# Kernel tuning notes

Hardware: AMD Instinct MI355X
Metric: run time of the kernel (lower is better)

The kernel has to match this reference:

```python
import jax, jax.numpy as jnp
import numpy as np

B, N, M = 64, 256, 16
H_A = 256
DMIN, DMAX, STEP = 0.0, 3.0, 0.2
N_FILTERS = 16  # arange(0, 3.0+0.2, 0.2) -> 16 gaussians, == h_b
N_CONV = 3
N_CLASSES = 6
IN_DIM = 2 * H_A + N_FILTERS  # 528
EPS = 1e-5


def _bn(x, gamma, beta):
    # BatchNorm1d in training mode: batch stats over all but last axis, biased var
    axes = tuple(range(x.ndim - 1))
    mu = jnp.mean(x, axis=axes, keepdims=True)
    var = jnp.var(x, axis=axes, keepdims=True)
    return (x - mu) * jax.lax.rsqrt(var + EPS) * gamma + beta


def setup_inputs() -> dict:
    key = jax.random.key(0)
    ks = jax.random.split(key, 10)
    nbr_adj_dist = jax.random.uniform(ks[0], (B, N, M), dtype=jnp.float32) * DMAX
    nbr_adj_list = jax.random.randint(ks[1], (B, N, M), 0, N, dtype=jnp.int32)
    emb_table = jax.random.normal(ks[2], (N, H_A), dtype=jnp.float32)
    s = 1.0 / np.sqrt(IN_DIM)
    W_full = jax.random.uniform(ks[3], (N_CONV, IN_DIM, 2 * H_A), minval=-s, maxval=s, dtype=jnp.float32)
    b_full = jax.random.uniform(ks[4], (N_CONV, 2 * H_A), minval=-s, maxval=s, dtype=jnp.float32)
    g_h = jnp.ones((N_CONV, 2 * H_A), jnp.float32)
    beta_h = jnp.zeros((N_CONV, 2 * H_A), jnp.float32)
    g_o = jnp.ones((N_CONV, H_A), jnp.float32)
    beta_o = jnp.zeros((N_CONV, H_A), jnp.float32)
    sc = 1.0 / np.sqrt(H_A)
    W_cls = jax.random.uniform(ks[5], (H_A, N_CLASSES), minval=-sc, maxval=sc, dtype=jnp.float32)
    b_cls = jax.random.uniform(ks[6], (N_CLASSES,), minval=-sc, maxval=sc, dtype=jnp.float32)
    return {"nbr_adj_dist": nbr_adj_dist, "nbr_adj_list": nbr_adj_list,
            "emb_table": emb_table, "W_full": W_full, "b_full": b_full,
            "g_h": g_h, "beta_h": beta_h, "g_o": g_o, "beta_o": beta_o,
            "W_cls": W_cls, "b_cls": b_cls}


def reference(nbr_adj_dist, nbr_adj_list, emb_table, W_full, b_full,
              g_h, beta_h, g_o, beta_o, W_cls, b_cls):
    # Gaussian distance expansion -> bond embedding [B,N,M,h_b]
    filters = jnp.arange(DMIN, DMAX + STEP, STEP, dtype=jnp.float32)
    nbr_emb = jnp.exp(-((nbr_adj_dist[..., None] - filters) ** 2) / (STEP ** 2))

    # atom embedding of arange(N), broadcast over batch -> [B,N,h_a]
    atom_emb = jnp.broadcast_to(emb_table[None], (B, N, H_A))

    idx = nbr_adj_list.reshape(B, N * M, 1)
    for l in range(N_CONV):
        # gather neighbor atom embeddings [B,N,M,h_a]
        atom_nbr = jnp.take_along_axis(atom_emb, idx, axis=1).reshape(B, N, M, H_A)
        self_emb = jnp.broadcast_to(atom_emb[:, :, None, :], (B, N, M, H_A))
        total = jnp.concatenate([self_emb, atom_nbr, nbr_emb], axis=-1)  # [B,N,M,528]
        z = jnp.einsum('bnmi,io->bnmo', total, W_full[l]) + b_full[l]
        z = _bn(z, g_h[l], beta_h[l])
        nbr_filter, nbr_core = jnp.split(z, 2, axis=-1)
        nbr_sumed = jnp.sum(jax.nn.sigmoid(nbr_filter) * jax.nn.relu(nbr_core), axis=2)
        nbr_sumed = _bn(nbr_sumed, g_o[l], beta_o[l])
        atom_emb = jax.nn.relu(atom_emb + nbr_sumed)

    atom_emb = jax.nn.relu(atom_emb)
    pooled = jnp.sum(atom_emb, axis=1) / N  # pooling by num_atoms
    logits = pooled @ W_cls + b_cls
    return jax.nn.softmax(logits, axis=-1)
```

## Files before the change

kernel.cpp:

```cpp
#include <hip/hip_runtime.h>
#include <math.h>

#define NB 64
#define NA 256
#define NM 16
#define HA 256
#define NF 16
#define NCONV 3
#define NCLS 6
#define EPSB 1e-5f

typedef __attribute__((ext_vector_type(8))) short short8v;
typedef __attribute__((ext_vector_type(4))) float f32x4;

__device__ __forceinline__ short f2bf(float x) {
  union { float f; unsigned u; } v; v.f = x;
  unsigned r = v.u + 0x7fff + ((v.u >> 16) & 1);
  return (short)(r >> 16);
}

__global__ void prep_weights(const float* __restrict__ Wf,
                             short* __restrict__ WT, short* __restrict__ W3bf) {
  int i = blockIdx.x * 256 + threadIdx.x;
  const int TOT1 = NCONV * 1024 * 256;
  if (i < TOT1) {
    int l = i / (1024 * 256);
    int r = i - l * (1024 * 256);
    int o = r >> 8, k = r & 255;
    float w = (o < 512) ? Wf[(l * 528 + k) * 512 + o]
                        : Wf[(l * 528 + 256 + k) * 512 + (o - 512)];
    WT[i] = f2bf(w);
  }
  const int TOT2 = NCONV * 512 * NF;
  if (i < TOT2) {
    int l = i / (512 * NF);
    int r = i - l * (512 * NF);
    int o = r >> 4, k = r & 15;
    W3bf[i] = f2bf(Wf[(l * 528 + 512 + k) * 512 + o]);
  }
}

__global__ void gauss_kernel(const float* __restrict__ dist, short* __restrict__ Gbf) {
  int i = blockIdx.x * 256 + threadIdx.x;
  int r = i >> 4, f = i & 15;
  float d = dist[r];
  float x = d - 0.2f * (float)f;
  Gbf[i] = f2bf(__expf(-x * x * 25.0f));
}

__global__ void init_atom(const float* __restrict__ emb, float* __restrict__ atom) {
  int i = blockIdx.x * 256 + threadIdx.x;
  atom[i] = emb[i & (NA * HA - 1)];
}

__global__ void emb_bf(const float* __restrict__ emb, short* __restrict__ ebf) {
  int i = blockIdx.x * 256 + threadIdx.x;
  ebf[i] = f2bf(emb[i]);
}

__global__ __launch_bounds__(256) void gemm_mfma(const short* __restrict__ Abf,
                                                 const short* __restrict__ WT,
                                                 float* __restrict__ C, int Mrows) {
  __shared__ short As[128][72];
  __shared__ short Bs[128][72];
  int t = threadIdx.x;
  int wave = t >> 6, lane = t & 63;
  int wr = wave >> 1, wc = wave & 1;
  int l16 = lane & 15, lhi = lane >> 4;

  int wg = blockIdx.x;
  int nRowBlocks = Mrows >> 7;
  int rowBlock, colBlock;
  if (nRowBlocks >= 8) {
    rowBlock = (wg & 7) + ((wg >> 6) << 3);
    colBlock = (wg >> 3) & 7;
  } else {
    rowBlock = wg % nRowBlocks;
    colBlock = wg / nRowBlocks;
  }
  int rowBase = rowBlock << 7, colBase = colBlock << 7;

  f32x4 acc[4][4];
#pragma unroll
  for (int i = 0; i < 4; ++i)
#pragma unroll
    for (int j = 0; j < 4; ++j) acc[i][j] = (f32x4)(0.f);

  for (int k0 = 0; k0 < 256; k0 += 64) {
#pragma unroll
    for (int cc = 0; cc < 4; ++cc) {
      int c = t + cc * 256;
      int row = c >> 3, ko = (c & 7) << 3;
      *(int4*)&As[row][ko] = *(const int4*)&Abf[(size_t)(rowBase + row) * 256 + k0 + ko];
      *(int4*)&Bs[row][ko] = *(const int4*)&WT[(size_t)(colBase + row) * 256 + k0 + ko];
    }
    __syncthreads();
#pragma unroll
    for (int ks = 0; ks < 2; ++ks) {
      int kk = ks * 32 + lhi * 8;
      short8v a[4], b[4];
#pragma unroll
      for (int f = 0; f < 4; ++f) {
        a[f] = *(const short8v*)&As[wr * 64 + f * 16 + l16][kk];
        b[f] = *(const short8v*)&Bs[wc * 64 + f * 16 + l16][kk];
      }
#pragma unroll
      for (int i = 0; i < 4; ++i)
#pragma unroll
        for (int j = 0; j < 4; ++j)
          acc[i][j] = __builtin_amdgcn_mfma_f32_16x16x32_bf16(a[i], b[j], acc[i][j], 0, 0, 0);
    }
    __syncthreads();
  }
#pragma unroll
  for (int i = 0; i < 4; ++i) {
#pragma unroll
    for (int j = 0; j < 4; ++j) {
      int col = colBase + wc * 64 + j * 16 + l16;
      int row0 = rowBase + wr * 64 + i * 16 + lhi * 4;
#pragma unroll
      for (int r = 0; r < 4; ++r)
        C[(size_t)(row0 + r) * 1024 + col] = acc[i][j][r];
    }
  }
}

__device__ __forceinline__ void decode_wg(int wg, int& b, int& n0) {
  int x = wg & 7;
  int t2 = wg >> 3;
  int ng = t2 & 31;
  int bhi = t2 >> 5;
  b = bhi * 8 + x;
  n0 = ng * 8;
}

template <int PASS>
__global__ __launch_bounds__(256, 2) void pass_mfma(const float* __restrict__ H,
                                                    const short* __restrict__ Gbf,
                                                    const int* __restrict__ adj,
                                                    const short* __restrict__ W3bf,
                                                    const float* __restrict__ coef,
                                                    float* __restrict__ nbr,
                                                    float* __restrict__ stats,
                                                    int batched) {
  __shared__ short Gb[128][40];
  __shared__ short W3t[512][40];
  __shared__ float x1s[8][512];
  __shared__ int jis[128];
  __shared__ float cf[1024];

  int t = threadIdx.x;
  int b, n0;
  decode_wg(blockIdx.x, b, n0);
  int hbase = batched ? b * NA : 0;

#pragma unroll
  for (int c = 0; c < 2; ++c) {
    int col = t * 2 + c;
    const int4* src = (const int4*)&W3bf[(size_t)col * 16];
    *(int4*)&W3t[col][0] = src[0];
    *(int4*)&W3t[col][8] = src[1];
    *(int4*)&W3t[col][16] = make_int4(0, 0, 0, 0);
    *(int4*)&W3t[col][24] = make_int4(0, 0, 0, 0);
  }
  if (t < 128) {
    const int4* src = (const int4*)&Gbf[((size_t)(b * NA + n0) * NM + t) * NF];
    *(int4*)&Gb[t][0] = src[0];
    *(int4*)&Gb[t][8] = src[1];
    *(int4*)&Gb[t][16] = make_int4(0, 0, 0, 0);
    *(int4*)&Gb[t][24] = make_int4(0, 0, 0, 0);
    jis[t] = adj[(b * NA + n0) * NM + t];
  }
  {
    int nn = t >> 5, c0 = (t & 31) * 16;
    const float4* src = (const float4*)&H[(size_t)(hbase + n0 + nn) * 1024 + c0];
    float4* dst = (float4*)&x1s[nn][c0];
    dst[0] = src[0]; dst[1] = src[1]; dst[2] = src[2]; dst[3] = src[3];
  }
  if (PASS == 1) {
    cf[t] = coef[t]; cf[256 + t] = coef[256 + t];
    cf[512 + t] = coef[512 + t]; cf[768 + t] = coef[768 + t];
  }
  __syncthreads();

  int lane = t & 63, wv = t >> 6;
  int l16 = lane & 15, lhi = lane >> 4;

  short8v bf[8];
  int oc[8];
#pragma unroll
  for (int j = 0; j < 8; ++j) {
    int col = wv * 64 + (j & 3) * 16 + l16 + ((j >= 4) ? 256 : 0);
    oc[j] = col;
    bf[j] = *(const short8v*)&W3t[col][lhi * 8];
  }

  float scf[4], shf[4], scc[4], shc[4];
  if (PASS == 1) {
#pragma unroll
    for (int p = 0; p < 4; ++p) {
      scf[p] = cf[oc[p]];       shf[p] = cf[512 + oc[p]];
      scc[p] = cf[oc[p + 4]];   shc[p] = cf[512 + oc[p + 4]];
    }
  }

  float s1f[4] = {0, 0, 0, 0}, s2f[4] = {0, 0, 0, 0};
  float s1c[4] = {0, 0, 0, 0}, s2c[4] = {0, 0, 0, 0};
  float sB1[4] = {0, 0, 0, 0}, sB2[4] = {0, 0, 0, 0};

  for (int h = 0; h < 2; ++h) {
    f32x4 acc[4][8];
#pragma unroll
    for (int f = 0; f < 4; ++f)
#pragma unroll
      for (int j = 0; j < 8; ++j) acc[f][j] = (f32x4)(0.f);
    short8v af[4];
#pragma unroll
    for (int f = 0; f < 4; ++f)
      af[f] = *(const short8v*)&Gb[(h * 4 + f) * 16 + l16][lhi * 8];
#pragma unroll
    for (int f = 0; f < 4; ++f)
#pragma unroll
      for (int j = 0; j < 8; ++j)
        acc[f][j] = __builtin_amdgcn_mfma_f32_16x16x32_bf16(af[f], bf[j], acc[f][j], 0, 0, 0);

#pragma unroll
    for (int f = 0; f < 4; ++f) {
      int nn = h * 4 + f;
      int n = n0 + nn;
      int jv[4];
#pragma unroll
      for (int r = 0; r < 4; ++r) jv[r] = jis[nn * 16 + lhi * 4 + r];
      float yv[8][4];
#pragma unroll
      for (int j = 0; j < 8; ++j)
#pragma unroll
        for (int r = 0; r < 4; ++r)
          yv[j][r] = H[(size_t)(hbase + jv[r]) * 1024 + 512 + oc[j]];
      float x1v[8];
#pragma unroll
      for (int j = 0; j < 8; ++j) x1v[j] = x1s[nn][oc[j]];

      if (PASS == 0) {
#pragma unroll
        for (int p = 0; p < 4; ++p) {
#pragma unroll
          for (int r = 0; r < 4; ++r) {
            float zf = acc[f][p][r] + x1v[p] + yv[p][r];
            float zc = acc[f][p + 4][r] + x1v[p + 4] + yv[p + 4][r];
            s1f[p] += zf; s2f[p] = fmaf(zf, zf, s2f[p]);
            s1c[p] += zc; s2c[p] = fmaf(zc, zc, s2c[p]);
          }
        }
      } else {
#pragma unroll
        for (int p = 0; p < 4; ++p) {
          float ps = 0.f;
#pragma unroll
          for (int r = 0; r < 4; ++r) {
            float zf = acc[f][p][r] + x1v[p] + yv[p][r];
            float zc = acc[f][p + 4][r] + x1v[p + 4] + yv[p + 4][r];
            float yfv = fmaf(zf, scf[p], shf[p]);
            float ycv = fmaf(zc, scc[p], shc[p]);
            float sig = 1.0f / (1.0f + __expf(-yfv));
            ps = fmaf(sig, fmaxf(ycv, 0.f), ps);
          }
          ps += __shfl_xor(ps, 16);
          ps += __shfl_xor(ps, 32);
          if (lhi == 0) {
            nbr[(size_t)(b * NA + n) * HA + oc[p]] = ps;
            sB1[p] += ps; sB2[p] = fmaf(ps, ps, sB2[p]);
          }
        }
      }
    }
  }

  if (PASS == 0) {
#pragma unroll
    for (int p = 0; p < 4; ++p) {
      float v;
      v = s1f[p]; v += __shfl_xor(v, 16); v += __shfl_xor(v, 32);
      if (lhi == 0) atomicAdd(&stats[oc[p]], v);
      v = s2f[p]; v += __shfl_xor(v, 16); v += __shfl_xor(v, 32);
      if (lhi == 0) atomicAdd(&stats[512 + oc[p]], v);
      v = s1c[p]; v += __shfl_xor(v, 16); v += __shfl_xor(v, 32);
      if (lhi == 0) atomicAdd(&stats[oc[p + 4]], v);
      v = s2c[p]; v += __shfl_xor(v, 16); v += __shfl_xor(v, 32);
      if (lhi == 0) atomicAdd(&stats[512 + oc[p + 4]], v);
    }
  } else {
#pragma unroll
    for (int p = 0; p < 4; ++p) {
      if (lhi == 0) {
        atomicAdd(&stats[oc[p]], sB1[p]);
        atomicAdd(&stats[256 + oc[p]], sB2[p]);
      }
    }
  }
}

__global__ void finalize1(const float* __restrict__ bn1, const float* __restrict__ g,
                          const float* __restrict__ beta, float* __restrict__ coef) {
  int t = threadIdx.x;
  const float inv = 1.0f / (float)(NB * NA * NM);
  float mu = bn1[t] * inv;
  float var = bn1[512 + t] * inv - mu * mu;
  float sc = g[t] * rsqrtf(var + EPSB);
  coef[t] = sc;
  coef[512 + t] = beta[t] - mu * sc;
}

__global__ void finalize2(const float* __restrict__ bn2, const float* __restrict__ g,
                          const float* __restrict__ beta, float* __restrict__ coef2) {
  int t = threadIdx.x;
  const float inv = 1.0f / (float)(NB * NA);
  float mu = bn2[t] * inv;
  float var = bn2[256 + t] * inv - mu * mu;
  float sc = g[t] * rsqrtf(var + EPSB);
  coef2[t] = sc;
  coef2[256 + t] = beta[t] - mu * sc;
}

__global__ void pass_c(float4* __restrict__ atom, const float4* __restrict__ nbr,
                       const float* __restrict__ coef2, short* __restrict__ abf) {
  int i = blockIdx.x * 256 + threadIdx.x;
  int o = (i & 63) * 4;
  float4 a = atom[i];
  float4 nv = nbr[i];
  a.x = fmaxf(a.x + fmaf(nv.x, coef2[o + 0], coef2[256 + o + 0]), 0.f);
  a.y = fmaxf(a.y + fmaf(nv.y, coef2[o + 1], coef2[256 + o + 1]), 0.f);
  a.z = fmaxf(a.z + fmaf(nv.z, coef2[o + 2], coef2[256 + o + 2]), 0.f);
  a.w = fmaxf(a.w + fmaf(nv.w, coef2[o + 3], coef2[256 + o + 3]), 0.f);
  atom[i] = a;
  short4 s;
  s.x = f2bf(a.x); s.y = f2bf(a.y); s.z = f2bf(a.z); s.w = f2bf(a.w);
  *(short4*)&abf[(size_t)i * 4] = s;
}

__global__ __launch_bounds__(256) void epilogue(const float* __restrict__ atom,
                                                const float* __restrict__ Wc,
                                                const float* __restrict__ bc,
                                                float* __restrict__ out) {
  __shared__ float pooled[HA];
  __shared__ float lg[NCLS];
  int b = blockIdx.x, t = threadIdx.x;
  float s = 0.f;
  for (int n = 0; n < NA; ++n) s += atom[(size_t)(b * NA + n) * HA + t];
  pooled[t] = s * (1.0f / (float)NA);
  __syncthreads();
  if (t < NCLS) {
    float a = bc[t];
    for (int o = 0; o < HA; ++o) a += pooled[o] * Wc[o * NCLS + t];
    lg[t] = a;
  }
  __syncthreads();
  if (t == 0) {
    float mx = lg[0];
    for (int c = 1; c < NCLS; ++c) mx = fmaxf(mx, lg[c]);
    float e[NCLS], den = 0.f;
    for (int c = 0; c < NCLS; ++c) { e[c] = __expf(lg[c] - mx); den += e[c]; }
    for (int c = 0; c < NCLS; ++c) out[b * NCLS + c] = e[c] / den;
  }
}

extern "C" void kernel_launch(void* const* d_in, const int* in_sizes, int n_in,
                              void* d_out, int out_size, void* d_ws, size_t ws_size,
                              hipStream_t stream) {
  const float* dist = (const float*)d_in[0];
  const int* adj = (const int*)d_in[1];
  const float* emb = (const float*)d_in[2];
  const float* Wf = (const float*)d_in[3];
  const float* gh = (const float*)d_in[5];
  const float* bh = (const float*)d_in[6];
  const float* go = (const float*)d_in[7];
  const float* bo = (const float*)d_in[8];
  const float* Wc = (const float*)d_in[9];
  const float* bc = (const float*)d_in[10];
  float* out = (float*)d_out;

  char* p = (char*)d_ws;
  short* Gbf = (short*)p;   p += (size_t)NB * NA * NM * NF * 2;
  float* H = (float*)p;     p += (size_t)NB * NA * 1024 * 4;
  float* H0 = (float*)p;    p += (size_t)NA * 1024 * 4;
  float* atom = (float*)p;  p += (size_t)NB * NA * HA * 4;
  float* nbr = (float*)p;   p += (size_t)NB * NA * HA * 4;
  short* WT = (short*)p;    p += (size_t)NCONV * 1024 * 256 * 2;
  short* Abf = (short*)p;   p += (size_t)NB * NA * 256 * 2;
  short* Ebf = (short*)p;   p += (size_t)NA * 256 * 2;
  short* W3bf = (short*)p;  p += (size_t)NCONV * 512 * NF * 2;
  float* bn1 = (float*)p;   p += 1024 * 4;
  float* bn2 = (float*)p;   p += 512 * 4;
  float* coef1 = (float*)p; p += 1024 * 4;
  float* coef2 = (float*)p; p += 512 * 4;

  prep_weights<<<3072, 256, 0, stream>>>(Wf, WT, W3bf);
  gauss_kernel<<<16384, 256, 0, stream>>>(dist, Gbf);
  init_atom<<<16384, 256, 0, stream>>>(emb, atom);
  emb_bf<<<256, 256, 0, stream>>>(emb, Ebf);

  for (int l = 0; l < NCONV; ++l) {
    hipMemsetAsync(bn1, 0, (1024 + 512) * 4, stream);
    int Mrows = (l == 0) ? NA : NB * NA;
    const short* Amat = (l == 0) ? Ebf : Abf;
    float* Hl = (l == 0) ? H0 : H;
    gemm_mfma<<<(Mrows / 128) * 8, 256, 0, stream>>>(Amat, WT + (size_t)l * 1024 * 256, Hl, Mrows);
    pass_mfma<0><<<2048, 256, 0, stream>>>(Hl, Gbf, adj, W3bf + (size_t)l * 512 * NF,
                                           nullptr, nullptr, bn1, l > 0);
    finalize1<<<1, 512, 0, stream>>>(bn1, gh + l * 512, bh + l * 512, coef1);
    pass_mfma<1><<<2048, 256, 0, stream>>>(Hl, Gbf, adj, W3bf + (size_t)l * 512 * NF,
                                           coef1, nbr, bn2, l > 0);
    finalize2<<<1, 256, 0, stream>>>(bn2, go + l * 256, bo + l * 256, coef2);
    pass_c<<<4096, 256, 0, stream>>>((float4*)atom, (const float4*)nbr, coef2, Abf);
  }
  epilogue<<<NB, 256, 0, stream>>>(atom, Wc, bc, out);
}
```

Before: 571.9 us.

## Drop LDS staging in pass kernel, load fragments directly and process one atom per iteration

Removes the shared-memory staging of the Gaussian features, the W3 slice and the self rows of H. MFMA operands are now loaded straight from global memory, with zero-padding done in registers. The loop handles one atom at a time with 8 accumulators instead of 32, and launch bounds go from 2 to 3 blocks per SIMD. The aim is lower LDS use and register pressure to raise occupancy, traded against more uncached global reads per block and shorter MFMA batches.

```diff
diff --git a/kernel.cpp b/kernel.cpp
--- a/kernel.cpp
+++ b/kernel.cpp
@@ -135,7 +135,7 @@
 }
 
 template <int PASS>
-__global__ __launch_bounds__(256, 2) void pass_mfma(const float* __restrict__ H,
+__global__ __launch_bounds__(256, 3) void pass_mfma(const float* __restrict__ H,
                                                     const short* __restrict__ Gbf,
                                                     const int* __restrict__ adj,
                                                     const short* __restrict__ W3bf,
@@ -143,9 +143,6 @@
                                                     float* __restrict__ nbr,
                                                     float* __restrict__ stats,
                                                     int batched) {
-  __shared__ short Gb[128][40];
-  __shared__ short W3t[512][40];
-  __shared__ float x1s[8][512];
   __shared__ int jis[128];
   __shared__ float cf[1024];
 
@@ -154,29 +151,7 @@
   decode_wg(blockIdx.x, b, n0);
   int hbase = batched ? b * NA : 0;
 
-#pragma unroll
-  for (int c = 0; c < 2; ++c) {
-    int col = t * 2 + c;
-    const int4* src = (const int4*)&W3bf[(size_t)col * 16];
-    *(int4*)&W3t[col][0] = src[0];
-    *(int4*)&W3t[col][8] = src[1];
-    *(int4*)&W3t[col][16] = make_int4(0, 0, 0, 0);
-    *(int4*)&W3t[col][24] = make_int4(0, 0, 0, 0);
-  }
-  if (t < 128) {
-    const int4* src = (const int4*)&Gbf[((size_t)(b * NA + n0) * NM + t) * NF];
-    *(int4*)&Gb[t][0] = src[0];
-    *(int4*)&Gb[t][8] = src[1];
-    *(int4*)&Gb[t][16] = make_int4(0, 0, 0, 0);
-    *(int4*)&Gb[t][24] = make_int4(0, 0, 0, 0);
-    jis[t] = adj[(b * NA + n0) * NM + t];
-  }
-  {
-    int nn = t >> 5, c0 = (t & 31) * 16;
-    const float4* src = (const float4*)&H[(size_t)(hbase + n0 + nn) * 1024 + c0];
-    float4* dst = (float4*)&x1s[nn][c0];
-    dst[0] = src[0]; dst[1] = src[1]; dst[2] = src[2]; dst[3] = src[3];
-  }
+  if (t < 128) jis[t] = adj[(b * NA + n0) * NM + t];
   if (PASS == 1) {
     cf[t] = coef[t]; cf[256 + t] = coef[256 + t];
     cf[512 + t] = coef[512 + t]; cf[768 + t] = coef[768 + t];
@@ -185,14 +160,15 @@
 
   int lane = t & 63, wv = t >> 6;
   int l16 = lane & 15, lhi = lane >> 4;
-
-  short8v bf[8];
+  const short8v zv = {0, 0, 0, 0, 0, 0, 0, 0};
+
+  short8v bfm[8];
   int oc[8];
 #pragma unroll
   for (int j = 0; j < 8; ++j) {
     int col = wv * 64 + (j & 3) * 16 + l16 + ((j >= 4) ? 256 : 0);
     oc[j] = col;
-    bf[j] = *(const short8v*)&W3t[col][lhi * 8];
+    bfm[j] = (lhi < 2) ? *(const short8v*)&W3bf[(size_t)col * NF + lhi * 8] : zv;
   }
 
   float scf[4], shf[4], scc[4], shc[4];
@@ -208,69 +184,61 @@
   float s1c[4] = {0, 0, 0, 0}, s2c[4] = {0, 0, 0, 0};
   float sB1[4] = {0, 0, 0, 0}, sB2[4] = {0, 0, 0, 0};
 
-  for (int h = 0; h < 2; ++h) {
-    f32x4 acc[4][8];
-#pragma unroll
-    for (int f = 0; f < 4; ++f)
-#pragma unroll
-      for (int j = 0; j < 8; ++j) acc[f][j] = (f32x4)(0.f);
-    short8v af[4];
-#pragma unroll
-    for (int f = 0; f < 4; ++f)
-      af[f] = *(const short8v*)&Gb[(h * 4 + f) * 16 + l16][lhi * 8];
-#pragma unroll
-    for (int f = 0; f < 4; ++f)
-#pragma unroll
-      for (int j = 0; j < 8; ++j)
-        acc[f][j] = __builtin_amdgcn_mfma_f32_16x16x32_bf16(af[f], bf[j], acc[f][j], 0, 0, 0);
-
-#pragma unroll
-    for (int f = 0; f < 4; ++f) {
-      int nn = h * 4 + f;
-      int n = n0 + nn;
-      int jv[4];
-#pragma unroll
-      for (int r = 0; r < 4; ++r) jv[r] = jis[nn * 16 + lhi * 4 + r];
-      float yv[8][4];
-#pragma unroll
-      for (int j = 0; j < 8; ++j)
-#pragma unroll
-        for (int r = 0; r < 4; ++r)
-          yv[j][r] = H[(size_t)(hbase + jv[r]) * 1024 + 512 + oc[j]];
-      float x1v[8];
-#pragma unroll
-      for (int j = 0; j < 8; ++j) x1v[j] = x1s[nn][oc[j]];
-
-      if (PASS == 0) {
-#pragma unroll
-        for (int p = 0; p < 4; ++p) {
-#pragma unroll
-          for (int r = 0; r < 4; ++r) {
-            float zf = acc[f][p][r] + x1v[p] + yv[p][r];
-            float zc = acc[f][p + 4][r] + x1v[p + 4] + yv[p + 4][r];
-            s1f[p] += zf; s2f[p] = fmaf(zf, zf, s2f[p]);
-            s1c[p] += zc; s2c[p] = fmaf(zc, zc, s2c[p]);
-          }
+  for (int nn = 0; nn < 8; ++nn) {
+    int n = n0 + nn;
+    short8v af = (lhi < 2)
+        ? *(const short8v*)&Gbf[(((size_t)(b * NA + n)) * NM + l16) * NF + lhi * 8]
+        : zv;
+    f32x4 acc[8];
+#pragma unroll
+    for (int j = 0; j < 8; ++j) acc[j] = (f32x4)(0.f);
+#pragma unroll
+    for (int j = 0; j < 8; ++j)
+      acc[j] = __builtin_amdgcn_mfma_f32_16x16x32_bf16(af, bfm[j], acc[j], 0, 0, 0);
+
+    int jv[4];
+#pragma unroll
+    for (int r = 0; r < 4; ++r) jv[r] = jis[nn * 16 + lhi * 4 + r];
+    const float* hs = &H[(size_t)(hbase + n) * 1024];
+    float x1v[8];
+#pragma unroll
+    for (int j = 0; j < 8; ++j) x1v[j] = hs[oc[j]];
+    float yv[8][4];
+#pragma unroll
+    for (int j = 0; j < 8; ++j)
+#pragma unroll
+      for (int r = 0; r < 4; ++r)
+        yv[j][r] = H[(size_t)(hbase + jv[r]) * 1024 + 512 + oc[j]];
+
+    if (PASS == 0) {
+#pragma unroll
+      for (int p = 0; p < 4; ++p) {
+#pragma unroll
+        for (int r = 0; r < 4; ++r) {
+          float zf = acc[p][r] + x1v[p] + yv[p][r];
+          float zc = acc[p + 4][r] + x1v[p + 4] + yv[p + 4][r];
+          s1f[p] += zf; s2f[p] = fmaf(zf, zf, s2f[p]);
+          s1c[p] += zc; s2c[p] = fmaf(zc, zc, s2c[p]);
         }
-      } else {
-#pragma unroll
-        for (int p = 0; p < 4; ++p) {
-          float ps = 0.f;
-#pragma unroll
-          for (int r = 0; r < 4; ++r) {
-            float zf = acc[f][p][r] + x1v[p] + yv[p][r];
-            float zc = acc[f][p + 4][r] + x1v[p + 4] + yv[p + 4][r];
-            float yfv = fmaf(zf, scf[p], shf[p]);
-            float ycv = fmaf(zc, scc[p], shc[p]);
-            float sig = 1.0f / (1.0f + __expf(-yfv));
-            ps = fmaf(sig, fmaxf(ycv, 0.f), ps);
-          }
-          ps += __shfl_xor(ps, 16);
-          ps += __shfl_xor(ps, 32);
-          if (lhi == 0) {
-            nbr[(size_t)(b * NA + n) * HA + oc[p]] = ps;
-            sB1[p] += ps; sB2[p] = fmaf(ps, ps, sB2[p]);
-          }
+      }
+    } else {
+#pragma unroll
+      for (int p = 0; p < 4; ++p) {
+        float ps = 0.f;
+#pragma unroll
+        for (int r = 0; r < 4; ++r) {
+          float zf = acc[p][r] + x1v[p] + yv[p][r];
+          float zc = acc[p + 4][r] + x1v[p + 4] + yv[p + 4][r];
+          float yfv = fmaf(zf, scf[p], shf[p]);
+          float ycv = fmaf(zc, scc[p], shc[p]);
+          float sig = 1.0f / (1.0f + __expf(-yfv));
+          ps = fmaf(sig, fmaxf(ycv, 0.f), ps);
+        }
+        ps += __shfl_xor(ps, 16);
+        ps += __shfl_xor(ps, 32);
+        if (lhi == 0) {
+          nbr[(size_t)(b * NA + n) * HA + oc[p]] = ps;
+          sB1[p] += ps; sB2[p] = fmaf(ps, ps, sB2[p]);
         }
       }
     }
```

Result: faster. 546.4 us (-4.5%).
